# Performance work log

Measured on AMD Instinct MI355X. Metric: run time of the kernel, lower is better.

The kernel has to match this reference:

```python
import jax, jax.numpy as jnp
import numpy as np

D_MODEL = 512
STATE_DIM = 6
D_STATE = 16
D_CONV = 4
EXPAND = 2
D_INNER = EXPAND * D_MODEL            # 1024
DT_RANK = -(-D_MODEL // 16)           # ceil(d_model/16) = 32


def setup_inputs() -> dict:
    key = jax.random.key(0)
    ks = jax.random.split(key, 12)
    s = 0.02
    return {
        "features": jax.random.normal(ks[0], (32, 2048, D_MODEL), dtype=jnp.float32),
        # Mamba params (mamba_ssm defaults: in/out_proj bias=False, conv+dt_proj bias=True)
        "in_proj_w": jax.random.normal(ks[1], (2 * D_INNER, D_MODEL), dtype=jnp.float32) * s,
        "conv_w": jax.random.normal(ks[2], (D_INNER, D_CONV), dtype=jnp.float32) * s,
        "conv_b": jnp.zeros((D_INNER,), dtype=jnp.float32),
        "x_proj_w": jax.random.normal(ks[3], (DT_RANK + 2 * D_STATE, D_INNER), dtype=jnp.float32) * s,
        "dt_proj_w": jax.random.normal(ks[4], (D_INNER, DT_RANK), dtype=jnp.float32) * s,
        "dt_proj_b": jax.random.normal(ks[5], (D_INNER,), dtype=jnp.float32) * s,
        "A_log": jnp.log(jnp.broadcast_to(jnp.arange(1, D_STATE + 1, dtype=jnp.float32), (D_INNER, D_STATE))),
        "D": jnp.ones((D_INNER,), dtype=jnp.float32),
        "out_proj_w": jax.random.normal(ks[6], (D_MODEL, D_INNER), dtype=jnp.float32) * s,
        # trailing fc head: d_model -> state_dim**2
        "fc_w": jax.random.normal(ks[7], (STATE_DIM * STATE_DIM, D_MODEL), dtype=jnp.float32) * s,
        "fc_b": jnp.zeros((STATE_DIM * STATE_DIM,), dtype=jnp.float32),
    }


def reference(features, in_proj_w, conv_w, conv_b, x_proj_w, dt_proj_w, dt_proj_b,
              A_log, D, out_proj_w, fc_w, fc_b):
    # Original loops Mamba over timesteps with seq_len=1 slices -> each timestep is
    # independent. Flatten (batch, seq) into one token axis and vectorize.
    B_, T, dm = features.shape
    f = features.reshape(B_ * T, dm)                      # (N, d_model)

    xz = f @ in_proj_w.T                                  # (N, 2*d_inner)
    x, z = jnp.split(xz, 2, axis=-1)
    # causal depthwise conv on a length-1 sequence: only the last tap contributes
    x = jax.nn.silu(x * conv_w[:, -1] + conv_b)           # (N, d_inner)

    x_dbl = x @ x_proj_w.T                                # (N, dt_rank + 2*d_state)
    dt = x_dbl[:, :DT_RANK]
    Bm = x_dbl[:, DT_RANK:DT_RANK + D_STATE]              # (N, d_state)
    Cm = x_dbl[:, DT_RANK + D_STATE:]                     # (N, d_state)
    delta = jax.nn.softplus(dt @ dt_proj_w.T + dt_proj_b) # (N, d_inner)

    # single-step selective scan with h0 = 0:
    #   h = exp(delta*A)*0 + delta*B*x ;  y = sum_s C_s h_s + D*x
    # (A_log therefore never affects the output for seq_len=1 calls)
    bc = jnp.sum(Bm * Cm, axis=-1, keepdims=True)         # (N, 1)
    y = delta * x * bc + D * x                            # (N, d_inner)
    y = y * jax.nn.silu(z)

    out = y @ out_proj_w.T                                # (N, d_model)
    A_flat = out @ fc_w.T + fc_b                          # (N, state_dim**2)
    return A_flat.reshape(B_, T, STATE_DIM, STATE_DIM)
```

## Files before the change

kernel.cpp:

```cpp
#include <hip/hip_runtime.h>

typedef unsigned short u16;
typedef unsigned int u32;
typedef __attribute__((ext_vector_type(8))) short bf16x8;
typedef __attribute__((ext_vector_type(4))) float f32x4;

#define NTOK 65536
#define DM 512
#define DI 1024

__device__ __forceinline__ float bf2f(u16 u){ u32 x=((u32)u)<<16; float f; __builtin_memcpy(&f,&x,4); return f; }
__device__ __forceinline__ u16 f2bf(float f){ u32 u; __builtin_memcpy(&u,&f,4); u += 0x7fffu + ((u>>16)&1u); return (u16)(u>>16); }
__device__ __forceinline__ float siluf(float x){ return x/(1.f+__expf(-x)); }
__device__ __forceinline__ float softplus_fast(float x){
  float l = __logf(1.f + __expf(x));
  return (x > 20.f) ? x : l;
}

__device__ __forceinline__ void gload_lds16(const void* g, void* l){
  __builtin_amdgcn_global_load_lds((const __attribute__((address_space(1))) u32*)g,
                                   (__attribute__((address_space(3))) u32*)l, 16, 0, 0);
}

__global__ void k_sentinel(float* out){ out[0] = 1.2345e6f; }

__global__ void k_cast_bf16(const float* __restrict__ in, u16* __restrict__ out, int n){
  int i = (blockIdx.x*256 + threadIdx.x)*4;
  if (i >= n) return;
  float4 v = *(const float4*)(in + i);
  ushort4 o; o.x=f2bf(v.x); o.y=f2bf(v.y); o.z=f2bf(v.z); o.w=f2bf(v.w);
  *(ushort4*)(out + i) = o;
}

__global__ void k_make_wa(const float* __restrict__ fcw, const float* __restrict__ opw,
                          u16* __restrict__ wa){
  int j = blockIdx.x*256 + threadIdx.x;
  int i = blockIdx.y;
  float s = 0.f;
  if (i < 36){
    const float* fr = fcw + i*DM;
    #pragma unroll 8
    for (int k=0;k<DM;++k) s += fr[k]*opw[(size_t)k*DI + j];
  }
  wa[(size_t)i*DI + j] = f2bf(s);
}

__global__ __launch_bounds__(512) void k_gemm_xz(
  const u16* __restrict__ A, const u16* __restrict__ B,
  const float* __restrict__ convw, const float* __restrict__ convb,
  u16* __restrict__ xp, u16* __restrict__ zs)
{
  __shared__ u16 smem[36864];
  const int tid=threadIdx.x, wv=tid>>6, ln=tid&63;
  const int l15=ln&15, l4=ln>>4;
  const int d=blockIdx.x, xcd=d&7, q=d>>3;
  const int g = xcd + 8*(q>>3);
  const int cb = q & 7;
  const int r0 = g*128, c0 = cb*256;
  const int wm=wv>>2, wn=wv&3;
  f32x4 acc[4][4]={};

  const int arow=(wv&1)*64+ln, achk=wv>>1;
  const int brow=(wv&3)*64+ln, bch=wv>>2;
  const u16* Ag  = A + (size_t)(r0+arow)*DM + achk*8;
  const u16* Bg0 = B + (size_t)(c0+brow)*DM + (bch+0)*8;
  const u16* Bg1 = B + (size_t)(c0+brow)*DM + (bch+2)*8;
  const int ldsA = wv*512;
  const int ldsB0 = wv*512, ldsB1 = 4096 + wv*512;

  auto STAGE=[&](int buf, int kt){
    const int k0 = kt*32;
    u16* Ad = smem + buf*12288;
    u16* Bd = Ad + 4096;
    gload_lds16(Ag  + k0, Ad + ldsA);
    gload_lds16(Bg0 + k0, Bd + ldsB0);
    gload_lds16(Bg1 + k0, Bd + ldsB1);
  };

  int offA[4], offB[4];
  #pragma unroll
  for (int m=0;m<4;++m) offA[m] = l4*1024 + (wm*64 + m*16 + l15)*8;
  #pragma unroll
  for (int n=0;n<4;++n) offB[n] = l4*2048 + (wn*64 + n*16 + l15)*8;

  STAGE(0,0); STAGE(1,1);
  #pragma clang loop unroll(disable)
  for (int t=0;t<16;++t){
    __builtin_amdgcn_sched_barrier(0);
    if (t<15) asm volatile("s_waitcnt vmcnt(3)" ::: "memory");
    else      asm volatile("s_waitcnt vmcnt(0)" ::: "memory");
    __builtin_amdgcn_s_barrier();
    __builtin_amdgcn_sched_barrier(0);
    if (t+2<16) STAGE((t+2)%3, t+2);
    const u16* Ac = smem + (t%3)*12288;
    const u16* Bc = Ac + 4096;
    bf16x8 af[4], bfr[4];
    #pragma unroll
    for (int m=0;m<4;++m) af[m]=*(const bf16x8*)(Ac + offA[m]);
    #pragma unroll
    for (int n=0;n<4;++n) bfr[n]=*(const bf16x8*)(Bc + offB[n]);
    #pragma unroll
    for (int m=0;m<4;++m)
      #pragma unroll
      for (int n=0;n<4;++n)
        acc[m][n]=__builtin_amdgcn_mfma_f32_16x16x32_bf16(af[m],bfr[n],acc[m][n],0,0,0);
    __builtin_amdgcn_sched_barrier(0);
  }
  __syncthreads();

  const bool isx = (c0 < DI);
  u16* W = smem;
  #pragma unroll
  for (int ch=0; ch<2; ++ch){
    if ((wn>>1) == ch){
      #pragma unroll
      for (int n=0;n<4;++n){
        int tcol = (wn&1)*64 + n*16 + l15;
        int gcol = c0 + ch*128 + tcol;
        float cw = isx ? convw[gcol*4+3] : 0.f;
        float cbv= isx ? convb[gcol]     : 0.f;
        #pragma unroll
        for (int m=0;m<4;++m){
          int trow = wm*64 + m*16 + l4*4;
          #pragma unroll
          for (int r=0;r<4;++r){
            float v = acc[m][n][r];
            float o = isx ? siluf(v*cw + cbv) : siluf(v);
            W[(trow+r)*136 + tcol] = f2bf(o);
          }
        }
      }
    }
    __syncthreads();
    const int orow = tid>>2, qq = tid&3;
    const u16* sp = W + orow*136 + qq*32;
    const int gc = c0 + ch*128 + qq*32;
    u16* dst = (isx ? xp : zs) + (size_t)(r0+orow)*DI + (isx ? gc : gc - DI);
    #pragma unroll
    for (int j=0;j<4;++j)
      ((int4*)dst)[j] = ((const int4*)sp)[j];
    __syncthreads();
  }
}

template<int EPI>
__global__ __launch_bounds__(256) void k_gemm_n64(
  const u16* __restrict__ A, const u16* __restrict__ B,
  u16* __restrict__ dtb, float* __restrict__ bc,
  const float* __restrict__ fcb, float* __restrict__ out)
{
  __shared__ u16 smem[24576];
  u16* SA = smem;
  u16* SB = smem + 16384;
  const int tid=threadIdx.x, wv=tid>>6, ln=tid&63;
  const int l15=ln&15, l4=ln>>4, h=l15&7;
  const int r0=blockIdx.x*128;
  const int wm=wv>>1, wn=wv&1;
  const int sr=ln>>3, scs=((ln&7)^sr)*8;
  const int chk0=(l4^h)*8, chk1=((l4+4)^h)*8;
  const int rA=(wm*64+l15)*64, rB=(wn*32+l15)*64;
  f32x4 acc[4][2]={};

  auto STAGE=[&](int buf, int k0){
    u16* Ad = SA + buf*8192;
    u16* Bd = SB + buf*4096;
    #pragma unroll
    for (int it=0;it<4;++it){
      int c=wv*4+it;
      gload_lds16(A + (size_t)(r0 + c*8 + sr)*DI + k0 + scs, Ad + c*512);
    }
    #pragma unroll
    for (int it=0;it<2;++it){
      int c=wv*2+it;
      gload_lds16(B + (size_t)(c*8 + sr)*DI + k0 + scs, Bd + c*512);
    }
  };

  STAGE(0, 0);
  __syncthreads();
  __builtin_amdgcn_sched_barrier(0);
  int cur = 0;
  #pragma clang loop unroll(disable)
  for (int t=0;t<16;++t){
    if (t < 15) STAGE(cur^1, (t+1)*64);
    const u16* Ac = SA + cur*8192;
    const u16* Bc = SB + cur*4096;
    #pragma unroll
    for (int kk=0;kk<2;++kk){
      const int ch = kk ? chk1 : chk0;
      bf16x8 af[4], bfr[2];
      #pragma unroll
      for (int m=0;m<4;++m) af[m]=*(const bf16x8*)(Ac + rA + m*1024 + ch);
      #pragma unroll
      for (int n=0;n<2;++n) bfr[n]=*(const bf16x8*)(Bc + rB + n*1024 + ch);
      #pragma unroll
      for (int m=0;m<4;++m)
        #pragma unroll
        for (int n=0;n<2;++n)
          acc[m][n]=__builtin_amdgcn_mfma_f32_16x16x32_bf16(af[m],bfr[n],acc[m][n],0,0,0);
    }
    __syncthreads();
    __builtin_amdgcn_sched_barrier(0);
    cur ^= 1;
  }

  if (EPI==0){
    float* W = (float*)smem;
    #pragma unroll
    for (int n=0;n<2;++n){
      int j = wn*32 + n*16 + l15;
      #pragma unroll
      for (int m=0;m<4;++m){
        int trow = wm*64 + m*16 + l4*4;
        #pragma unroll
        for (int r=0;r<4;++r)
          W[(trow+r)*68 + j] = acc[m][n][r];
      }
    }
    __syncthreads();
    const int row = tid>>1, half = tid&1;
    const float* wr = W + row*68;
    if (half==0){
      u16* dst = dtb + (size_t)(r0+row)*32;
      #pragma unroll
      for (int qv=0;qv<4;++qv){
        bf16x8 o;
        #pragma unroll
        for (int e=0;e<8;++e) o[e] = (short)f2bf(wr[qv*8+e]);
        *(bf16x8*)(dst + qv*8) = o;
      }
    } else {
      float s=0.f;
      #pragma unroll
      for (int e=0;e<16;++e) s += wr[32+e]*wr[48+e];
      bc[r0+row] = s;
    }
  } else {
    #pragma unroll
    for (int n=0;n<2;++n){
      int j = wn*32 + n*16 + l15;
      #pragma unroll
      for (int m=0;m<4;++m){
        #pragma unroll
        for (int r=0;r<4;++r){
          int t = r0 + wm*64 + m*16 + l4*4 + r;
          if (j < 36) out[(size_t)t*36 + j] = acc[m][n][r] + fcb[j];
        }
      }
    }
  }
}

__global__ __launch_bounds__(256) void k_delta_y(
  const u16* __restrict__ dtb, const u16* __restrict__ Bw,
  const float* __restrict__ dpb, const float* __restrict__ Dv,
  const float* __restrict__ bc,
  const u16* __restrict__ xp, u16* __restrict__ zy)
{
  __shared__ u16 smem[17408];
  u16* As = smem;
  u16* Bs = smem + 4096;
  const int tid=threadIdx.x, wv=tid>>6, ln=tid&63;
  const int l15=ln&15, l4=ln>>4;
  const int c0=blockIdx.x*128, r0=blockIdx.y*128;
  const int wm=wv>>1, wn=wv&1;
  const int sr=ln>>2, sc=(ln&3)*8;
  #pragma unroll
  for (int it=0;it<2;++it){
    int c=wv*2+it;
    gload_lds16(dtb + (size_t)(r0 + c*16 + sr)*32 + sc, As + c*512);
  }
  #pragma unroll
  for (int it=0;it<2;++it){
    int c=wv*2+it;
    gload_lds16(Bw + (size_t)(c0 + c*16 + sr)*32 + sc, Bs + c*512);
  }
  __syncthreads();
  __builtin_amdgcn_sched_barrier(0);
  f32x4 acc[4][4]={};
  bf16x8 af[4], bfr[4];
  #pragma unroll
  for (int m=0;m<4;++m) af[m]=*(const bf16x8*)(As + (wm*64+m*16+l15)*32 + l4*8);
  #pragma unroll
  for (int n=0;n<4;++n) bfr[n]=*(const bf16x8*)(Bs + (wn*64+n*16+l15)*32 + l4*8);
  #pragma unroll
  for (int m=0;m<4;++m)
    #pragma unroll
    for (int n=0;n<4;++n)
      acc[m][n]=__builtin_amdgcn_mfma_f32_16x16x32_bf16(af[m],bfr[n],acc[m][n],0,0,0);
  __syncthreads();
  u16* W = smem;
  #pragma unroll
  for (int n=0;n<4;++n){
    int tcol = wn*64 + n*16 + l15;
    int j = c0 + tcol;
    float dpbj = dpb[j], Dj = Dv[j];
    #pragma unroll
    for (int m=0;m<4;++m){
      int trow = wm*64 + m*16 + l4*4;
      #pragma unroll
      for (int r=0;r<4;++r){
        float delta = softplus_fast(acc[m][n][r] + dpbj);
        float w = delta*bc[r0 + trow + r] + Dj;
        W[(trow+r)*136 + tcol] = f2bf(w);
      }
    }
  }
  __syncthreads();
  const int row = tid>>1, half = tid&1;
  const u16* wp = W + row*136 + half*64;
  const size_t gbase = (size_t)(r0 + row)*DI + c0 + half*64;
  const u16* xpp = xp + gbase;
  u16* zp = zy + gbase;
  #pragma unroll
  for (int q=0;q<8;++q){
    bf16x8 wv8 = *(const bf16x8*)(wp + q*8);
    bf16x8 xv  = *(const bf16x8*)(xpp + q*8);
    bf16x8 zv  = *(const bf16x8*)(zp + q*8);
    bf16x8 ov;
    #pragma unroll
    for (int e=0;e<8;++e){
      float y = bf2f((u16)wv8[e]) * bf2f((u16)xv[e]) * bf2f((u16)zv[e]);
      ov[e] = (short)f2bf(y);
    }
    *(bf16x8*)(zp + q*8) = ov;
  }
}

extern "C" void kernel_launch(void* const* d_in, const int* in_sizes, int n_in,
                              void* d_out, int out_size, void* d_ws, size_t ws_size,
                              hipStream_t stream){
  const float* f      = (const float*)d_in[0];
  const float* inpw   = (const float*)d_in[1];
  const float* convw  = (const float*)d_in[2];
  const float* convb  = (const float*)d_in[3];
  const float* xprojw = (const float*)d_in[4];
  const float* dtpw   = (const float*)d_in[5];
  const float* dtpb   = (const float*)d_in[6];
  const float* Dv     = (const float*)d_in[8];
  const float* opw    = (const float*)d_in[9];
  const float* fcw    = (const float*)d_in[10];
  const float* fcb    = (const float*)d_in[11];
  float* out = (float*)d_out;

  char* ws = (char*)d_ws;
  size_t off = 0;
  auto alloc = [&](size_t sz)->void*{ void* p = ws + off; off += (sz + 255) & ~(size_t)255; return p; };
  u16*   fbf = (u16*)  alloc((size_t)NTOK*DM*2);
  u16*   xp  = (u16*)  alloc((size_t)NTOK*DI*2);
  u16*   zy  = (u16*)  alloc((size_t)NTOK*DI*2);
  u16*   dtb = (u16*)  alloc((size_t)NTOK*32*2);
  float* bc  = (float*)alloc((size_t)NTOK*4);
  u16*   ipw = (u16*)  alloc((size_t)2048*512*2);
  u16*   xpw = (u16*)  alloc((size_t)64*1024*2);
  u16*   dpw = (u16*)  alloc((size_t)1024*32*2);
  u16*   wa  = (u16*)  alloc((size_t)64*1024*2);
  if (off > ws_size){ k_sentinel<<<1,1,0,stream>>>(out); return; }

  k_cast_bf16<<<dim3((NTOK*DM/4)/256),256,0,stream>>>(f, fbf, NTOK*DM);
  k_cast_bf16<<<dim3((2048*512/4)/256),256,0,stream>>>(inpw, ipw, 2048*512);
  k_cast_bf16<<<dim3((64*1024/4)/256),256,0,stream>>>(xprojw, xpw, 64*1024);
  k_cast_bf16<<<dim3((1024*32/4)/256),256,0,stream>>>(dtpw, dpw, 1024*32);
  k_make_wa<<<dim3(4,64),256,0,stream>>>(fcw, opw, wa);

  k_gemm_xz<<<dim3(4096),512,0,stream>>>(fbf, ipw, convw, convb, xp, zy);
  k_gemm_n64<0><<<dim3(512),256,0,stream>>>(xp, xpw, dtb, bc, nullptr, nullptr);
  k_delta_y<<<dim3(8,512),256,0,stream>>>(dtb, dpw, dtpb, Dv, bc, xp, zy);
  k_gemm_n64<1><<<dim3(512),256,0,stream>>>(zy, wa, nullptr, nullptr, fcb, out);
}
```

Measured before the change: 555.8 us.

## Enlarge in_proj GEMM tile to 256x256 with four-stage LDS pipeline

The in_proj GEMM block tile grows from 128x256 to 256x256, so each wave now holds 8x4 MFMA accumulators and A/B reuse per LDS load goes up. The LDS ring grows from three to four buffers with prefetch distance three, and the wait counts are adjusted to match. The grid is halved to 2048 blocks, and the epilogue writes two row rounds per chunk. The aim is fewer global/LDS loads per FLOP and better latency hiding, at the cost of 128KB LDS, higher register pressure, and fewer blocks resident per CU.

```diff
diff --git a/kernel.cpp b/kernel.cpp
--- a/kernel.cpp
+++ b/kernel.cpp
@@ -45,62 +45,59 @@
   wa[(size_t)i*DI + j] = f2bf(s);
 }
 
-__global__ __launch_bounds__(512) void k_gemm_xz(
+__global__ __launch_bounds__(512,2) void k_gemm_xz(
   const u16* __restrict__ A, const u16* __restrict__ B,
   const float* __restrict__ convw, const float* __restrict__ convb,
   u16* __restrict__ xp, u16* __restrict__ zs)
 {
-  __shared__ u16 smem[36864];
+  __shared__ u16 smem[65536];
   const int tid=threadIdx.x, wv=tid>>6, ln=tid&63;
   const int l15=ln&15, l4=ln>>4;
   const int d=blockIdx.x, xcd=d&7, q=d>>3;
   const int g = xcd + 8*(q>>3);
   const int cb = q & 7;
-  const int r0 = g*128, c0 = cb*256;
+  const int r0 = g*256, c0 = cb*256;
   const int wm=wv>>2, wn=wv&3;
-  f32x4 acc[4][4]={};
-
-  const int arow=(wv&1)*64+ln, achk=wv>>1;
-  const int brow=(wv&3)*64+ln, bch=wv>>2;
-  const u16* Ag  = A + (size_t)(r0+arow)*DM + achk*8;
-  const u16* Bg0 = B + (size_t)(c0+brow)*DM + (bch+0)*8;
-  const u16* Bg1 = B + (size_t)(c0+brow)*DM + (bch+2)*8;
-  const int ldsA = wv*512;
-  const int ldsB0 = wv*512, ldsB1 = 4096 + wv*512;
+  f32x4 acc[8][4]={};
+
+  const int ar = tid & 255, ah = tid >> 8;
+  const u16* Ag = A + (size_t)(r0+ar)*DM + ah*16;
+  const u16* Bg = B + (size_t)(c0+ar)*DM + ah*16;
+  const int ldsAd = (ah*2)*2048 + ar*8;
 
   auto STAGE=[&](int buf, int kt){
+    u16* Ls = smem + buf*16384;
     const int k0 = kt*32;
-    u16* Ad = smem + buf*12288;
-    u16* Bd = Ad + 4096;
-    gload_lds16(Ag  + k0, Ad + ldsA);
-    gload_lds16(Bg0 + k0, Bd + ldsB0);
-    gload_lds16(Bg1 + k0, Bd + ldsB1);
+    gload_lds16(Ag + k0,     Ls + ldsAd);
+    gload_lds16(Ag + k0 + 8, Ls + ldsAd + 2048);
+    gload_lds16(Bg + k0,     Ls + 8192 + ldsAd);
+    gload_lds16(Bg + k0 + 8, Ls + 8192 + ldsAd + 2048);
   };
 
-  int offA[4], offB[4];
-  #pragma unroll
-  for (int m=0;m<4;++m) offA[m] = l4*1024 + (wm*64 + m*16 + l15)*8;
-  #pragma unroll
-  for (int n=0;n<4;++n) offB[n] = l4*2048 + (wn*64 + n*16 + l15)*8;
-
-  STAGE(0,0); STAGE(1,1);
+  int offA[8], offB[4];
+  #pragma unroll
+  for (int m=0;m<8;++m) offA[m] = l4*2048 + (wm*128 + m*16 + l15)*8;
+  #pragma unroll
+  for (int n=0;n<4;++n) offB[n] = 8192 + l4*2048 + (wn*64 + n*16 + l15)*8;
+
+  STAGE(0,0); STAGE(1,1); STAGE(2,2);
   #pragma clang loop unroll(disable)
   for (int t=0;t<16;++t){
     __builtin_amdgcn_sched_barrier(0);
-    if (t<15) asm volatile("s_waitcnt vmcnt(3)" ::: "memory");
-    else      asm volatile("s_waitcnt vmcnt(0)" ::: "memory");
+    if (t<=13)      asm volatile("s_waitcnt vmcnt(8)" ::: "memory");
+    else if (t==14) asm volatile("s_waitcnt vmcnt(4)" ::: "memory");
+    else            asm volatile("s_waitcnt vmcnt(0)" ::: "memory");
     __builtin_amdgcn_s_barrier();
     __builtin_amdgcn_sched_barrier(0);
-    if (t+2<16) STAGE((t+2)%3, t+2);
-    const u16* Ac = smem + (t%3)*12288;
-    const u16* Bc = Ac + 4096;
-    bf16x8 af[4], bfr[4];
-    #pragma unroll
-    for (int m=0;m<4;++m) af[m]=*(const bf16x8*)(Ac + offA[m]);
-    #pragma unroll
-    for (int n=0;n<4;++n) bfr[n]=*(const bf16x8*)(Bc + offB[n]);
-    #pragma unroll
-    for (int m=0;m<4;++m)
+    if (t+3<16) STAGE((t+3)&3, t+3);
+    const u16* Ls = smem + (t&3)*16384;
+    bf16x8 af[8], bfr[4];
+    #pragma unroll
+    for (int m=0;m<8;++m) af[m]=*(const bf16x8*)(Ls + offA[m]);
+    #pragma unroll
+    for (int n=0;n<4;++n) bfr[n]=*(const bf16x8*)(Ls + offB[n]);
+    #pragma unroll
+    for (int m=0;m<8;++m)
       #pragma unroll
       for (int n=0;n<4;++n)
         acc[m][n]=__builtin_amdgcn_mfma_f32_16x16x32_bf16(af[m],bfr[n],acc[m][n],0,0,0);
@@ -117,11 +114,11 @@
       for (int n=0;n<4;++n){
         int tcol = (wn&1)*64 + n*16 + l15;
         int gcol = c0 + ch*128 + tcol;
-        float cw = isx ? convw[gcol*4+3] : 0.f;
-        float cbv= isx ? convb[gcol]     : 0.f;
-        #pragma unroll
-        for (int m=0;m<4;++m){
-          int trow = wm*64 + m*16 + l4*4;
+        float cw  = isx ? convw[gcol*4+3] : 0.f;
+        float cbv = isx ? convb[gcol]     : 0.f;
+        #pragma unroll
+        for (int m=0;m<8;++m){
+          int trow = wm*128 + m*16 + l4*4;
           #pragma unroll
           for (int r=0;r<4;++r){
             float v = acc[m][n][r];
@@ -132,13 +129,16 @@
       }
     }
     __syncthreads();
-    const int orow = tid>>2, qq = tid&3;
-    const u16* sp = W + orow*136 + qq*32;
-    const int gc = c0 + ch*128 + qq*32;
-    u16* dst = (isx ? xp : zs) + (size_t)(r0+orow)*DI + (isx ? gc : gc - DI);
-    #pragma unroll
-    for (int j=0;j<4;++j)
-      ((int4*)dst)[j] = ((const int4*)sp)[j];
+    #pragma unroll
+    for (int rnd=0;rnd<2;++rnd){
+      const int row = (tid>>2) + rnd*128, qq = tid&3;
+      const u16* sp = W + row*136 + qq*32;
+      const int gc = c0 + ch*128 + qq*32;
+      u16* dst = (isx ? xp : zs) + (size_t)(r0+row)*DI + (isx ? gc : gc - DI);
+      #pragma unroll
+      for (int j=0;j<4;++j)
+        ((int4*)dst)[j] = ((const int4*)sp)[j];
+    }
     __syncthreads();
   }
 }
@@ -363,7 +363,7 @@
   k_cast_bf16<<<dim3((1024*32/4)/256),256,0,stream>>>(dtpw, dpw, 1024*32);
   k_make_wa<<<dim3(4,64),256,0,stream>>>(fcw, opw, wa);
 
-  k_gemm_xz<<<dim3(4096),512,0,stream>>>(fbf, ipw, convw, convb, xp, zy);
+  k_gemm_xz<<<dim3(2048),512,0,stream>>>(fbf, ipw, convw, convb, xp, zy);
   k_gemm_n64<0><<<dim3(512),256,0,stream>>>(xp, xpw, dtb, bc, nullptr, nullptr);
   k_delta_y<<<dim3(8,512),256,0,stream>>>(dtb, dpw, dtpb, Dv, bc, xp, zy);
   k_gemm_n64<1><<<dim3(512),256,0,stream>>>(zy, wa, nullptr, nullptr, fcb, out);
```

Measured after the change: 675.5 us. 1.22x slower.
